# Optimization experiments

Hardware: AMD Instinct MI355X
Metric: run time of the kernel (lower is better)

## Reference

```python
import jax, jax.numpy as jnp
import numpy as np

# QLSTMClassifier (quantum mode): Embedding -> QLSTM (4 quantum gate layers per step) -> Linear -> log_softmax.
# NOTE: QLSTM.forward unbinds dim 0 (batch) and cats each x:(seq,emb) with hx:(batch,hid),
# which requires batch == seq_len. We honor that with S = batch = seq_len.
S = 256   # batch == seq_len
E = 1024  # embedding_dim
H = 10    # hidden_dim == n_qubits (required by f*cx elementwise product)
V = 50257 # vocab_size
T = 50    # tagset_size


def setup_inputs() -> dict:
    key = jax.random.key(0)
    ks = jax.random.split(key, 6)
    sentence = jax.random.randint(ks[0], (S, S), 0, V)                                   # (batch, seq)
    emb_table = jax.random.normal(ks[1], (V, E), jnp.float32) * 0.02                      # nn.Embedding weight
    Wg = jax.random.normal(ks[2], (4, E + H, H), jnp.float32) * (1.0 / np.sqrt(E + H))    # forget/input/update/output linears
    bg = jnp.zeros((4, H), jnp.float32)
    theta = jax.random.normal(ks[3], (4, H), jnp.float32)                                 # trainable RX angles per gate
    W_out = jax.random.normal(ks[4], (H, T), jnp.float32) * (1.0 / np.sqrt(H))            # hidden2tag
    b_out = jnp.zeros((T,), jnp.float32)
    return dict(sentence=sentence, emb_table=emb_table, Wg=Wg, bg=bg,
                theta=theta, W_out=W_out, b_out=b_out)


def _qlayer(z, th):
    # Exact closed form of the QLayer circuit on n wires starting from |0...0>:
    #   RX(z_w) then RX(th_w) on wire w  ==> RX(a_w) with a_w = z_w + th_w (product state),
    #   then CNOT ring: CNOT(0,1), CNOT(1,2), ..., CNOT(n-2,n-1), CNOT(n-1,0),
    # Heisenberg-picture pullback of Z_w through the CNOT ring gives
    #   M_0 = Z_1 Z_2 ... Z_{n-1},   M_w = Z_0 Z_1 ... Z_w  (w >= 1),
    # and on the product state <Z_j> = cos(a_j), so expectations factorize:
    #   out_0 = prod_{j>=1} cos(a_j),  out_w = prod_{j<=w} cos(a_j).
    c = jnp.cos(z + th)                                   # (B, H)
    cum = jnp.cumprod(c, axis=-1)                         # prefix products
    tail = jnp.prod(c[:, 1:], axis=-1, keepdims=True)     # wire-0 observable
    return jnp.concatenate([tail, cum[:, 1:]], axis=-1)   # (B, H)


def reference(sentence, emb_table, Wg, bg, theta, W_out, b_out):
    embeds = emb_table[sentence]                          # (S, S, E); scan axis = dim 0 (unbind dim)
    h0 = jnp.zeros((embeds.shape[0], theta.shape[1]), embeds.dtype)

    def step(carry, x):                                   # x: (S, E)
        hx, cx = carry
        comb = jnp.concatenate([x, hx], axis=-1)          # (S, E+H)
        z = jnp.einsum('bi,gio->gbo', comb, Wg) + bg[:, None, :]  # (4, S, H)
        f = jax.nn.sigmoid(_qlayer(z[0], theta[0]))
        i = jax.nn.sigmoid(_qlayer(z[1], theta[1]))
        g = jnp.tanh(_qlayer(z[2], theta[2]))
        o = jax.nn.sigmoid(_qlayer(z[3], theta[3]))
        cx = f * cx + i * g
        hx = o * jnp.tanh(cx)
        return (hx, cx), hx

    _, outs = jax.lax.scan(step, (h0, h0), embeds)        # (S, S, H)
    logits = outs @ W_out + b_out                         # (S, S, T)
    return jax.nn.log_softmax(logits, axis=2)
```

## Files before the change

### kernel.cpp

```cpp
#include <hip/hip_runtime.h>
#include <hip/hip_bf16.h>


#define E_DIM 1024
#define H_DIM 10
#define NC 40
#define V_DIM 50257
#define EHS 10340

typedef __attribute__((ext_vector_type(8))) short bf16x8;
typedef __attribute__((ext_vector_type(4))) float f32x4;

__device__ __forceinline__ unsigned short f2bf(float f) {
    unsigned u = __float_as_uint(f);
    unsigned r = u + 0x7FFFu + ((u >> 16) & 1u);
    return (unsigned short)(r >> 16);
}

__global__ __launch_bounds__(256) void k_wt(const float* __restrict__ Wg,
                                            unsigned short* __restrict__ Bfg) {
    int i = blockIdx.x * 256 + threadIdx.x;
    if (i >= 6144) return;
    int lane = i & 63, nt = (i >> 6) % 3, c = i / 192;
    int kg = lane >> 4, n = lane & 15;
    int nc = nt * 16 + n;
    unsigned short v[8];
#pragma unroll
    for (int j = 0; j < 8; ++j) {
        int k = c * 32 + kg * 8 + j;
        float w = 0.0f;
        if (nc < NC) {
            int g = nc / H_DIM, h = nc % H_DIM;
            w = Wg[g * EHS + k * H_DIM + h];
        }
        v[j] = f2bf(w);
    }
    bf16x8* dst = (bf16x8*)(Bfg + (size_t)i * 8);
    bf16x8 pk;
#pragma unroll
    for (int j = 0; j < 8; ++j) pk[j] = (short)v[j];
    *dst = pk;
}

__global__ __launch_bounds__(256, 4) void k_gemm(const float* __restrict__ emb,
                                                 const unsigned short* __restrict__ Bfg,
                                                 float* __restrict__ zu) {
    const int tid = threadIdx.x;
    const int wave = tid >> 6, lane = tid & 63;
    const int R0 = (blockIdx.x * 4 + wave) * 16;
    const int m = lane & 15, q = lane >> 4;

    int row = R0 + m;
    if (row > V_DIM - 1) row = V_DIM - 1;
    const float* arow = emb + (size_t)row * E_DIM + q * 8;

    f32x4 acc0 = {0.f, 0.f, 0.f, 0.f}, acc1 = acc0, acc2 = acc0;

#pragma unroll 2
    for (int c = 0; c < 32; ++c) {
        float4 a0 = *(const float4*)(arow + c * 32);
        float4 a1 = *(const float4*)(arow + c * 32 + 4);
        bf16x8 b0 = *(const bf16x8*)(Bfg + ((size_t)(c * 3 + 0) * 64 + lane) * 8);
        bf16x8 b1 = *(const bf16x8*)(Bfg + ((size_t)(c * 3 + 1) * 64 + lane) * 8);
        bf16x8 b2 = *(const bf16x8*)(Bfg + ((size_t)(c * 3 + 2) * 64 + lane) * 8);
        bf16x8 af;
        af[0] = (short)f2bf(a0.x); af[1] = (short)f2bf(a0.y);
        af[2] = (short)f2bf(a0.z); af[3] = (short)f2bf(a0.w);
        af[4] = (short)f2bf(a1.x); af[5] = (short)f2bf(a1.y);
        af[6] = (short)f2bf(a1.z); af[7] = (short)f2bf(a1.w);
        acc0 = __builtin_amdgcn_mfma_f32_16x16x32_bf16(af, b0, acc0, 0, 0, 0);
        acc1 = __builtin_amdgcn_mfma_f32_16x16x32_bf16(af, b1, acc1, 0, 0, 0);
        acc2 = __builtin_amdgcn_mfma_f32_16x16x32_bf16(af, b2, acc2, 0, 0, 0);
    }

    const int r0 = R0 + q * 4;
#pragma unroll
    for (int i = 0; i < 4; ++i) {
        int r = r0 + i;
        if (r < V_DIM) {
            size_t o = (size_t)r * NC;
            zu[o + m] = acc0[i];
            zu[o + 16 + m] = acc1[i];
            if (m < 8) zu[o + 32 + m] = acc2[i];
        }
    }
}

template <int CTRL>
__device__ __forceinline__ float dpp1(float x) {
    return __int_as_float(__builtin_amdgcn_update_dpp(
        __float_as_int(1.0f), __float_as_int(x), CTRL, 0xF, 0xF, false));
}
#define ROW_SHR(n) (0x110 + (n))
#define ROW_SHL(n) (0x100 + (n))

__device__ __forceinline__ float rdlane(float v, int l) {
    return __int_as_float(__builtin_amdgcn_readlane(__float_as_int(v), l));
}

__global__ __launch_bounds__(128) void k_rnn(const int* __restrict__ idx,
                                             const float* __restrict__ zu,
                                             const float* __restrict__ Wg,
                                             const float* __restrict__ bg,
                                             const float* __restrict__ theta,
                                             float* __restrict__ outs) {
    __shared__ float zbuf[2][640];
    __shared__ int toks[256];
    const int tid = threadIdx.x;
    const int b = blockIdx.x;

    if (tid >= 64) {
        const int p = tid - 64;
#pragma unroll
        for (int k = 0; k < 4; ++k) toks[p + k * 64] = idx[(p + k * 64) * 256 + b];
        const int j = p >> 2;
        const int s4 = p & 3;
        {
            int tv = toks[j];
            const float* src = zu + (size_t)tv * NC + s4 * 10;
            float* dst = &zbuf[0][j * 40 + s4 * 10];
#pragma unroll
            for (int e = 0; e < 5; ++e)
                *(float2*)(dst + 2 * e) = *(const float2*)(src + 2 * e);
        }
        __syncthreads();
        for (int blk = 0; blk < 16; ++blk) {
            if (blk + 1 < 16) {
                int tv = toks[(blk + 1) * 16 + j];
                const float* src = zu + (size_t)tv * NC + s4 * 10;
                float v[10];
#pragma unroll
                for (int e = 0; e < 5; ++e) {
                    float2 t2 = *(const float2*)(src + 2 * e);
                    v[2 * e] = t2.x; v[2 * e + 1] = t2.y;
                }
                float* dst = &zbuf[(blk + 1) & 1][j * 40 + s4 * 10];
#pragma unroll
                for (int e = 0; e < 5; ++e) {
                    float2 t2 = {v[2 * e], v[2 * e + 1]};
                    *(float2*)(dst + 2 * e) = t2;
                }
            }
            __syncthreads();
        }
    } else {
        const int lane = tid;
        const int r = lane >> 4;
        const int h = lane & 15;
        const int hc = (h < 10) ? h : 9;
        const int cidx = r * 10 + hc;

        float Wh[10];
#pragma unroll
        for (int j = 0; j < 10; ++j) Wh[j] = Wg[r * EHS + (E_DIM + j) * H_DIM + hc];
        const float bias = bg[cidx] + theta[cidx];

        const float kk = (r == 2) ? 2.0f : -1.0f;
        const float aa = (r == 2) ? 1.0f : 0.0f;
        const float bb = (r == 2) ? -2.0f : 1.0f;

        float cx = 0.0f, hx = 0.0f;
        __syncthreads();

        for (int blk = 0; blk < 16; ++blk) {
            const float* zb = zbuf[blk & 1];
            float zv = zb[cidx];
#pragma unroll 4
            for (int s = 0; s < 16; ++s) {
                float znext = zb[((s < 15) ? (s + 1) * 40 : s * 40) + cidx];

                float hv0 = rdlane(hx, 0), hv1 = rdlane(hx, 1), hv2 = rdlane(hx, 2),
                      hv3 = rdlane(hx, 3), hv4 = rdlane(hx, 4), hv5 = rdlane(hx, 5),
                      hv6 = rdlane(hx, 6), hv7 = rdlane(hx, 7), hv8 = rdlane(hx, 8),
                      hv9 = rdlane(hx, 9);
                float d0 = fmaf(hv0, Wh[0], fmaf(hv2, Wh[2],
                           fmaf(hv4, Wh[4], fmaf(hv6, Wh[6], hv8 * Wh[8]))));
                float d1 = fmaf(hv1, Wh[1], fmaf(hv3, Wh[3],
                           fmaf(hv5, Wh[5], fmaf(hv7, Wh[7], hv9 * Wh[9]))));
                float z = (zv + bias) + (d0 + d1);

                float cc = __builtin_amdgcn_cosf(z * 0.15915494309189535f);

                float pp = cc;
                pp *= dpp1<ROW_SHR(1)>(pp);
                pp *= dpp1<ROW_SHR(2)>(pp);
                pp *= dpp1<ROW_SHR(4)>(pp);
                pp *= dpp1<ROW_SHR(8)>(pp);
                float ss = (h < 10) ? cc : 1.0f;
                ss *= dpp1<ROW_SHL(1)>(ss);
                ss *= dpp1<ROW_SHL(2)>(ss);
                ss *= dpp1<ROW_SHL(4)>(ss);
                ss *= dpp1<ROW_SHL(8)>(ss);
                float tl = dpp1<ROW_SHL(1)>(ss);
                float qv = (h == 0) ? tl : pp;

                float e = __expf(kk * qv);
                float act = fmaf(bb, __builtin_amdgcn_rcpf(1.0f + e), aa);

                float fv = __shfl(act, h);
                float iv = __shfl(act, 16 + h);
                float gv = __shfl(act, 32 + h);
                float ov = __shfl(act, 48 + h);

                cx = fmaf(fv, cx, iv * gv);
                float e2 = __expf(2.0f * cx);
                float th = fmaf(-2.0f, __builtin_amdgcn_rcpf(1.0f + e2), 1.0f);
                hx = ov * th;

                int t = blk * 16 + s;
                if (lane < 10) outs[((size_t)t * 256 + b) * H_DIM + lane] = hx;
                zv = znext;
            }
            __syncthreads();
        }
    }
}

__global__ __launch_bounds__(256) void k_head(const float* __restrict__ outs,
                                              const float* __restrict__ Wo,
                                              const float* __restrict__ bo,
                                              float* __restrict__ out) {
    const size_t row = blockIdx.x * 256 + threadIdx.x;
    float hx[10];
#pragma unroll
    for (int i = 0; i < 5; ++i) {
        float2 v = *(const float2*)&outs[row * H_DIM + 2 * i];
        hx[2 * i] = v.x; hx[2 * i + 1] = v.y;
    }
    float lg[50];
#pragma unroll
    for (int cI = 0; cI < 50; ++cI) {
        float l = bo[cI];
#pragma unroll
        for (int j = 0; j < 10; ++j) l = fmaf(hx[j], Wo[j * 50 + cI], l);
        lg[cI] = l;
    }
    float m = lg[0];
#pragma unroll
    for (int cI = 1; cI < 50; ++cI) m = fmaxf(m, lg[cI]);
    float sum = 0.0f;
#pragma unroll
    for (int cI = 0; cI < 50; ++cI) sum += __expf(lg[cI] - m);
    float lse = m + __logf(sum);
#pragma unroll
    for (int i = 0; i < 25; ++i) {
        float2 v = {lg[2 * i] - lse, lg[2 * i + 1] - lse};
        *(float2*)&out[row * 50 + 2 * i] = v;
    }
}

extern "C" void kernel_launch(void* const* d_in, const int* in_sizes, int n_in,
                              void* d_out, int out_size, void* d_ws, size_t ws_size,
                              hipStream_t stream) {
    const int*   sentence = (const int*)d_in[0];
    const float* emb      = (const float*)d_in[1];
    const float* Wg       = (const float*)d_in[2];
    const float* bg       = (const float*)d_in[3];
    const float* theta    = (const float*)d_in[4];
    const float* Wo       = (const float*)d_in[5];
    const float* bo       = (const float*)d_in[6];
    float* out = (float*)d_out;

    float* ws = (float*)d_ws;
    unsigned short* Bfg = (unsigned short*)ws;
    float* zu   = ws + 24576;
    float* outs = zu + (size_t)V_DIM * NC;

    k_wt<<<24, 256, 0, stream>>>(Wg, Bfg);
    k_gemm<<<786, 256, 0, stream>>>(emb, Bfg, zu);
    k_rnn<<<256, 128, 0, stream>>>(sentence, zu, Wg, bg, theta, outs);
    k_head<<<256, 256, 0, stream>>>(outs, Wo, bo, out);
}
```

Measured before the change: 400.1 us.

## Preload all gate inputs into LDS up front and drop per-block recurrence syncs

The recurrent kernel used to run a producer/consumer split in which 64 threads streamed 16-step blocks of gathered gate pre-activations through a double buffer, with a block-wide barrier every 16 steps. Now all 128 threads gather the whole 256x40 slice into LDS (40 KB) before the loop. The recurrence wave then runs all 256 steps with no barriers. The GEMM's embedding-row loads also become nontemporal loads, to avoid polluting the cache with data that is streamed once. The trade-off is a larger up-front gather latency before the serial loop can start, plus higher LDS use per block.

```diff
diff --git a/kernel.cpp b/kernel.cpp
--- a/kernel.cpp
+++ b/kernel.cpp
@@ -58,16 +58,16 @@
 
 #pragma unroll 2
     for (int c = 0; c < 32; ++c) {
-        float4 a0 = *(const float4*)(arow + c * 32);
-        float4 a1 = *(const float4*)(arow + c * 32 + 4);
+        f32x4 a0 = __builtin_nontemporal_load((const f32x4*)(arow + c * 32));
+        f32x4 a1 = __builtin_nontemporal_load((const f32x4*)(arow + c * 32 + 4));
         bf16x8 b0 = *(const bf16x8*)(Bfg + ((size_t)(c * 3 + 0) * 64 + lane) * 8);
         bf16x8 b1 = *(const bf16x8*)(Bfg + ((size_t)(c * 3 + 1) * 64 + lane) * 8);
         bf16x8 b2 = *(const bf16x8*)(Bfg + ((size_t)(c * 3 + 2) * 64 + lane) * 8);
         bf16x8 af;
-        af[0] = (short)f2bf(a0.x); af[1] = (short)f2bf(a0.y);
-        af[2] = (short)f2bf(a0.z); af[3] = (short)f2bf(a0.w);
-        af[4] = (short)f2bf(a1.x); af[5] = (short)f2bf(a1.y);
-        af[6] = (short)f2bf(a1.z); af[7] = (short)f2bf(a1.w);
+        af[0] = (short)f2bf(a0[0]); af[1] = (short)f2bf(a0[1]);
+        af[2] = (short)f2bf(a0[2]); af[3] = (short)f2bf(a0[3]);
+        af[4] = (short)f2bf(a1[0]); af[5] = (short)f2bf(a1[1]);
+        af[6] = (short)f2bf(a1[2]); af[7] = (short)f2bf(a1[3]);
         acc0 = __builtin_amdgcn_mfma_f32_16x16x32_bf16(af, b0, acc0, 0, 0, 0);
         acc1 = __builtin_amdgcn_mfma_f32_16x16x32_bf16(af, b1, acc1, 0, 0, 0);
         acc2 = __builtin_amdgcn_mfma_f32_16x16x32_bf16(af, b2, acc2, 0, 0, 0);
@@ -104,115 +104,90 @@
                                              const float* __restrict__ bg,
                                              const float* __restrict__ theta,
                                              float* __restrict__ outs) {
-    __shared__ float zbuf[2][640];
-    __shared__ int toks[256];
+    __shared__ float zall[256 * NC];
     const int tid = threadIdx.x;
     const int b = blockIdx.x;
 
-    if (tid >= 64) {
-        const int p = tid - 64;
-#pragma unroll
-        for (int k = 0; k < 4; ++k) toks[p + k * 64] = idx[(p + k * 64) * 256 + b];
-        const int j = p >> 2;
-        const int s4 = p & 3;
-        {
-            int tv = toks[j];
-            const float* src = zu + (size_t)tv * NC + s4 * 10;
-            float* dst = &zbuf[0][j * 40 + s4 * 10];
+    {
+        const int j = tid >> 2;
+        const int qq = tid & 3;
+        int tok[8];
+#pragma unroll
+        for (int pass = 0; pass < 8; ++pass)
+            tok[pass] = idx[(size_t)(pass * 32 + j) * 256 + b];
+#pragma unroll
+        for (int pass = 0; pass < 8; ++pass) {
+            const float* src = zu + (size_t)tok[pass] * NC + qq * 10;
+            float* dst = &zall[(pass * 32 + j) * NC + qq * 10];
 #pragma unroll
             for (int e = 0; e < 5; ++e)
                 *(float2*)(dst + 2 * e) = *(const float2*)(src + 2 * e);
         }
-        __syncthreads();
-        for (int blk = 0; blk < 16; ++blk) {
-            if (blk + 1 < 16) {
-                int tv = toks[(blk + 1) * 16 + j];
-                const float* src = zu + (size_t)tv * NC + s4 * 10;
-                float v[10];
-#pragma unroll
-                for (int e = 0; e < 5; ++e) {
-                    float2 t2 = *(const float2*)(src + 2 * e);
-                    v[2 * e] = t2.x; v[2 * e + 1] = t2.y;
-                }
-                float* dst = &zbuf[(blk + 1) & 1][j * 40 + s4 * 10];
-#pragma unroll
-                for (int e = 0; e < 5; ++e) {
-                    float2 t2 = {v[2 * e], v[2 * e + 1]};
-                    *(float2*)(dst + 2 * e) = t2;
-                }
-            }
-            __syncthreads();
-        }
-    } else {
-        const int lane = tid;
-        const int r = lane >> 4;
-        const int h = lane & 15;
-        const int hc = (h < 10) ? h : 9;
-        const int cidx = r * 10 + hc;
-
-        float Wh[10];
-#pragma unroll
-        for (int j = 0; j < 10; ++j) Wh[j] = Wg[r * EHS + (E_DIM + j) * H_DIM + hc];
-        const float bias = bg[cidx] + theta[cidx];
-
-        const float kk = (r == 2) ? 2.0f : -1.0f;
-        const float aa = (r == 2) ? 1.0f : 0.0f;
-        const float bb = (r == 2) ? -2.0f : 1.0f;
-
-        float cx = 0.0f, hx = 0.0f;
-        __syncthreads();
-
-        for (int blk = 0; blk < 16; ++blk) {
-            const float* zb = zbuf[blk & 1];
-            float zv = zb[cidx];
-#pragma unroll 4
-            for (int s = 0; s < 16; ++s) {
-                float znext = zb[((s < 15) ? (s + 1) * 40 : s * 40) + cidx];
-
-                float hv0 = rdlane(hx, 0), hv1 = rdlane(hx, 1), hv2 = rdlane(hx, 2),
-                      hv3 = rdlane(hx, 3), hv4 = rdlane(hx, 4), hv5 = rdlane(hx, 5),
-                      hv6 = rdlane(hx, 6), hv7 = rdlane(hx, 7), hv8 = rdlane(hx, 8),
-                      hv9 = rdlane(hx, 9);
-                float d0 = fmaf(hv0, Wh[0], fmaf(hv2, Wh[2],
-                           fmaf(hv4, Wh[4], fmaf(hv6, Wh[6], hv8 * Wh[8]))));
-                float d1 = fmaf(hv1, Wh[1], fmaf(hv3, Wh[3],
-                           fmaf(hv5, Wh[5], fmaf(hv7, Wh[7], hv9 * Wh[9]))));
-                float z = (zv + bias) + (d0 + d1);
-
-                float cc = __builtin_amdgcn_cosf(z * 0.15915494309189535f);
-
-                float pp = cc;
-                pp *= dpp1<ROW_SHR(1)>(pp);
-                pp *= dpp1<ROW_SHR(2)>(pp);
-                pp *= dpp1<ROW_SHR(4)>(pp);
-                pp *= dpp1<ROW_SHR(8)>(pp);
-                float ss = (h < 10) ? cc : 1.0f;
-                ss *= dpp1<ROW_SHL(1)>(ss);
-                ss *= dpp1<ROW_SHL(2)>(ss);
-                ss *= dpp1<ROW_SHL(4)>(ss);
-                ss *= dpp1<ROW_SHL(8)>(ss);
-                float tl = dpp1<ROW_SHL(1)>(ss);
-                float qv = (h == 0) ? tl : pp;
-
-                float e = __expf(kk * qv);
-                float act = fmaf(bb, __builtin_amdgcn_rcpf(1.0f + e), aa);
-
-                float fv = __shfl(act, h);
-                float iv = __shfl(act, 16 + h);
-                float gv = __shfl(act, 32 + h);
-                float ov = __shfl(act, 48 + h);
-
-                cx = fmaf(fv, cx, iv * gv);
-                float e2 = __expf(2.0f * cx);
-                float th = fmaf(-2.0f, __builtin_amdgcn_rcpf(1.0f + e2), 1.0f);
-                hx = ov * th;
-
-                int t = blk * 16 + s;
-                if (lane < 10) outs[((size_t)t * 256 + b) * H_DIM + lane] = hx;
-                zv = znext;
-            }
-            __syncthreads();
-        }
+    }
+    __syncthreads();
+    if (tid >= 64) return;
+
+    const int lane = tid;
+    const int r = lane >> 4;
+    const int h = lane & 15;
+    const int hc = (h < 10) ? h : 9;
+    const int cidx = r * 10 + hc;
+
+    float Wh[10];
+#pragma unroll
+    for (int j = 0; j < 10; ++j) Wh[j] = Wg[r * EHS + (E_DIM + j) * H_DIM + hc];
+    const float bias = bg[cidx] + theta[cidx];
+
+    const float kk = (r == 2) ? 2.0f : -1.0f;
+    const float aa = (r == 2) ? 1.0f : 0.0f;
+    const float bb = (r == 2) ? -2.0f : 1.0f;
+
+    float cx = 0.0f, hx = 0.0f;
+    float zv = zall[cidx];
+#pragma unroll 8
+    for (int t = 0; t < 256; ++t) {
+        float znext = zall[((t < 255) ? (t + 1) : t) * NC + cidx];
+
+        float hv0 = rdlane(hx, 0), hv1 = rdlane(hx, 1), hv2 = rdlane(hx, 2),
+              hv3 = rdlane(hx, 3), hv4 = rdlane(hx, 4), hv5 = rdlane(hx, 5),
+              hv6 = rdlane(hx, 6), hv7 = rdlane(hx, 7), hv8 = rdlane(hx, 8),
+              hv9 = rdlane(hx, 9);
+        float d0 = fmaf(hv0, Wh[0], fmaf(hv2, Wh[2],
+                   fmaf(hv4, Wh[4], fmaf(hv6, Wh[6], hv8 * Wh[8]))));
+        float d1 = fmaf(hv1, Wh[1], fmaf(hv3, Wh[3],
+                   fmaf(hv5, Wh[5], fmaf(hv7, Wh[7], hv9 * Wh[9]))));
+        float z = (zv + bias) + (d0 + d1);
+
+        float cc = __builtin_amdgcn_cosf(z * 0.15915494309189535f);
+
+        float pp = cc;
+        pp *= dpp1<ROW_SHR(1)>(pp);
+        pp *= dpp1<ROW_SHR(2)>(pp);
+        pp *= dpp1<ROW_SHR(4)>(pp);
+        pp *= dpp1<ROW_SHR(8)>(pp);
+        float ss = (h < 10) ? cc : 1.0f;
+        ss *= dpp1<ROW_SHL(1)>(ss);
+        ss *= dpp1<ROW_SHL(2)>(ss);
+        ss *= dpp1<ROW_SHL(4)>(ss);
+        ss *= dpp1<ROW_SHL(8)>(ss);
+        float tl = dpp1<ROW_SHL(1)>(ss);
+        float qv = (h == 0) ? tl : pp;
+
+        float e = __expf(kk * qv);
+        float act = fmaf(bb, __builtin_amdgcn_rcpf(1.0f + e), aa);
+
+        float fv = __shfl(act, h);
+        float iv = __shfl(act, 16 + h);
+        float gv = __shfl(act, 32 + h);
+        float ov = __shfl(act, 48 + h);
+
+        cx = fmaf(fv, cx, iv * gv);
+        float e2 = __expf(2.0f * cx);
+        float th = fmaf(-2.0f, __builtin_amdgcn_rcpf(1.0f + e2), 1.0f);
+        hx = ov * th;
+
+        if (lane < 10) outs[((size_t)t * 256 + b) * H_DIM + lane] = hx;
+        zv = znext;
     }
 }
 
```

Result: faster. 387.1 us (-3.3%).
